# Optimization experiments

Hardware: AMD Instinct MI355X
Metric: run time of the kernel (lower is better)

The kernel has to match this reference:

```python
import jax, jax.numpy as jnp
import numpy as np

ALPHA = 1.0

def setup_inputs() -> dict:
    key = jax.random.key(0)
    k1, k2 = jax.random.split(key)
    B, T, F = 8, 4096, 1024
    x = jax.random.normal(k1, (B, T, F), dtype=jnp.float32)
    # ragged valid lengths in [T//2, T]; mask[b, t] = t < length[b]
    lengths = jax.random.randint(k2, (B,), T // 2, T + 1)
    attention_mask = (jnp.arange(T)[None, :] < lengths[:, None]).astype(jnp.int32)
    return {"input_values": x, "attention_mask": attention_mask}


def reference(input_values, attention_mask):
    # input_values: [B,T,F]; attention_mask: [B,T] (1 for valid, 0 for pad)
    m = attention_mask.astype(input_values.dtype)[..., None]          # [B,T,1]
    L = jnp.sum(m, axis=1)                                            # [B,1]
    # k: per-channel mean over valid timesteps (torch mean over dims [-1,-2])
    k = jnp.sum(input_values * m, axis=1) / L                         # [B,F]
    k_centered = k - jnp.mean(k, axis=-1, keepdims=True)              # [B,F] (center over channels)
    kd = jnp.sqrt(jnp.sum(k_centered ** 2, axis=-1, keepdims=True))   # [B,1]
    # center each timestep over channels
    x_centered = input_values - jnp.mean(input_values, axis=-1, keepdims=True)  # [B,T,F]
    qd = jnp.sqrt(jnp.sum(x_centered ** 2, axis=-1))                  # [B,T]
    num = jnp.einsum('btf,bf->bt', x_centered, k_centered)            # [B,T]
    C_qk = num / (qd * kd)                                            # [B,T]
    A = (1.0 - jax.nn.sigmoid(C_qk)) ** ALPHA                         # [B,T]
    # apply attention and zero out padded positions (original zero-pads)
    out = input_values * A[..., None] * m                             # [B,T,F]
    return out
```

## Files before the change

### kernel.cpp

```cpp
#include <hip/hip_runtime.h>
#include <math.h>

#define BB 8
#define TT 4096
#define FF 1024
#define F4 (FF / 4)
#define TS 128
#define TCHUNK (TT / TS)

typedef float vfloat4 __attribute__((ext_vector_type(4)));

__global__ __launch_bounds__(256) void k1_colsum(const float4* __restrict__ x4,
                                                 const int* __restrict__ mask,
                                                 float* __restrict__ ksum) {
    const int ts  = blockIdx.x;
    const int b   = blockIdx.y;
    const int tid = threadIdx.x;

    const int4* mrow = (const int4*)(mask + (size_t)b * TT + ts * TCHUNK);
    int nv = 0;
    #pragma unroll
    for (int i = 0; i < TCHUNK / 4; ++i) {
        int4 m = mrow[i];
        nv += m.x + m.y + m.z + m.w;
    }
    if (nv == 0) return;

    const float4* xb = x4 + ((size_t)b * TT + (size_t)ts * TCHUNK) * F4 + tid;
    float4 acc = make_float4(0.f, 0.f, 0.f, 0.f);
    #pragma unroll 8
    for (int t = 0; t < nv; ++t) {
        float4 v = xb[(size_t)t * F4];
        acc.x += v.x; acc.y += v.y; acc.z += v.z; acc.w += v.w;
    }

    float* dst = ksum + (size_t)b * FF + tid * 4;
    atomicAdd(dst + 0, acc.x);
    atomicAdd(dst + 1, acc.y);
    atomicAdd(dst + 2, acc.z);
    atomicAdd(dst + 3, acc.w);
}

__global__ __launch_bounds__(256) void k3_apply(const float4* __restrict__ x4,
                                                const int* __restrict__ mask,
                                                const float4* __restrict__ ksum4,
                                                float4* __restrict__ out4) {
    __shared__ float Lred[4];
    const int tid  = threadIdx.x;
    const int wave = tid >> 6;
    const int lane = tid & 63;
    const int b    = blockIdx.y;

    int c = 0;
    #pragma unroll
    for (int i = 0; i < 16; ++i) c += mask[(size_t)b * TT + tid + i * 256];
    float fc = (float)c;
    #pragma unroll
    for (int off = 32; off; off >>= 1) fc += __shfl_xor(fc, off);
    if (lane == 0) Lred[wave] = fc;
    __syncthreads();
    const float Lf   = Lred[0] + Lred[1] + Lred[2] + Lred[3];
    const float invL = 1.0f / Lf;

    const float4* krow = ksum4 + (size_t)b * F4;
    float4 kv[4];
    #pragma unroll
    for (int j = 0; j < 4; ++j) {
        kv[j] = krow[lane + 64 * j];
        kv[j].x *= invL; kv[j].y *= invL; kv[j].z *= invL; kv[j].w *= invL;
    }

    float a = 0.f, q = 0.f;
    #pragma unroll
    for (int j = 0; j < 4; ++j) {
        a += kv[j].x + kv[j].y + kv[j].z + kv[j].w;
        q = fmaf(kv[j].x, kv[j].x, fmaf(kv[j].y, kv[j].y,
            fmaf(kv[j].z, kv[j].z, fmaf(kv[j].w, kv[j].w, q))));
    }
    #pragma unroll
    for (int off = 32; off; off >>= 1) {
        a += __shfl_xor(a, off);
        q += __shfl_xor(q, off);
    }
    const float sk = a;
    const float kd = sqrtf(fmaxf(q - sk * sk * (1.0f / FF), 0.f));

    const int rowbase = blockIdx.x * 16 + wave * 4;
    const size_t base = ((size_t)b * TT + rowbase) * F4;

    const int4 m4 = *(const int4*)(mask + (size_t)b * TT + rowbase);
    const int  nv = m4.x + m4.y + m4.z + m4.w;

    for (int i = nv; i < 4; ++i) {
        vfloat4* orow = (vfloat4*)(out4 + base + (size_t)i * F4);
        vfloat4 z = (vfloat4)(0.f);
        #pragma unroll
        for (int j = 0; j < 4; ++j)
            __builtin_nontemporal_store(z, orow + lane + 64 * j);
    }
    if (nv == 0) return;

    float4 xn[4];
    #pragma unroll
    for (int j = 0; j < 4; ++j) xn[j] = (x4 + base)[lane + 64 * j];

    for (int i = 0; i < nv; ++i) {
        float4 xv[4];
        #pragma unroll
        for (int j = 0; j < 4; ++j) xv[j] = xn[j];
        if (i + 1 < nv) {
            const float4* xrow = x4 + base + (size_t)(i + 1) * F4;
            #pragma unroll
            for (int j = 0; j < 4; ++j) xn[j] = xrow[lane + 64 * j];
        }

        float s1 = 0.f, s2 = 0.f, s3 = 0.f;
        #pragma unroll
        for (int j = 0; j < 4; ++j) {
            s1 += xv[j].x + xv[j].y + xv[j].z + xv[j].w;
            s2 = fmaf(xv[j].x, xv[j].x, fmaf(xv[j].y, xv[j].y,
                 fmaf(xv[j].z, xv[j].z, fmaf(xv[j].w, xv[j].w, s2))));
            s3 = fmaf(xv[j].x, kv[j].x, fmaf(xv[j].y, kv[j].y,
                 fmaf(xv[j].z, kv[j].z, fmaf(xv[j].w, kv[j].w, s3))));
        }
        #pragma unroll
        for (int off = 32; off; off >>= 1) {
            s1 += __shfl_xor(s1, off);
            s2 += __shfl_xor(s2, off);
            s3 += __shfl_xor(s3, off);
        }

        const float mx  = s1 * (1.0f / FF);
        const float num = s3 - mx * sk;
        const float qd  = sqrtf(fmaxf(s2 - s1 * s1 * (1.0f / FF), 0.f));
        const float C   = num / (qd * kd);
        const float A   = 1.0f / (1.0f + __expf(C));

        vfloat4* orow = (vfloat4*)(out4 + base + (size_t)i * F4);
        #pragma unroll
        for (int j = 0; j < 4; ++j) {
            vfloat4 o;
            o.x = xv[j].x * A; o.y = xv[j].y * A;
            o.z = xv[j].z * A; o.w = xv[j].w * A;
            __builtin_nontemporal_store(o, orow + lane + 64 * j);
        }
    }
}

extern "C" void kernel_launch(void* const* d_in, const int* in_sizes, int n_in,
                              void* d_out, int out_size, void* d_ws, size_t ws_size,
                              hipStream_t stream) {
    const float* x    = (const float*)d_in[0];
    const int*   mask = (const int*)d_in[1];
    float*       out  = (float*)d_out;

    float* ksum = (float*)d_ws;

    hipMemsetAsync(ksum, 0, (size_t)BB * FF * sizeof(float), stream);

    k1_colsum<<<dim3(TS, BB), 256, 0, stream>>>((const float4*)x, mask, ksum);
    k3_apply<<<dim3(TT / 16, BB), 256, 0, stream>>>((const float4*)x, mask,
                                                    (const float4*)ksum,
                                                    (float4*)out);
}
```

Baseline: 247.7 us.

## Move padded-row zeroing and length count into the colsum kernel

The first kernel gains extra blocks. They write zeros to the padded output rows, and one extra block per batch counts the valid length and stores it to workspace. The zero stores can then overlap with the column-sum reads instead of sitting in the apply kernel. The apply kernel drops its per-block 4K-element mask reduction and the barrier that followed it. Blocks with no valid rows now exit before loading k, at the cost of one more workspace read per block.

```diff
diff --git a/kernel.cpp b/kernel.cpp
--- a/kernel.cpp
+++ b/kernel.cpp
@@ -7,60 +7,92 @@
 #define F4 (FF / 4)
 #define TS 128
 #define TCHUNK (TT / TS)
+#define ZB (TT / 16)
 
 typedef float vfloat4 __attribute__((ext_vector_type(4)));
 
 __global__ __launch_bounds__(256) void k1_colsum(const float4* __restrict__ x4,
                                                  const int* __restrict__ mask,
-                                                 float* __restrict__ ksum) {
-    const int ts  = blockIdx.x;
+                                                 float* __restrict__ ksum,
+                                                 float* __restrict__ Lf,
+                                                 float4* __restrict__ out4) {
+    const int bx  = blockIdx.x;
     const int b   = blockIdx.y;
     const int tid = threadIdx.x;
 
-    const int4* mrow = (const int4*)(mask + (size_t)b * TT + ts * TCHUNK);
-    int nv = 0;
-    #pragma unroll
-    for (int i = 0; i < TCHUNK / 4; ++i) {
-        int4 m = mrow[i];
-        nv += m.x + m.y + m.z + m.w;
-    }
-    if (nv == 0) return;
+    if (bx < TS) {
+        const int4* mrow = (const int4*)(mask + (size_t)b * TT + bx * TCHUNK);
+        int nv = 0;
+        #pragma unroll
+        for (int i = 0; i < TCHUNK / 4; ++i) {
+            int4 m = mrow[i];
+            nv += m.x + m.y + m.z + m.w;
+        }
+        if (nv == 0) return;
 
-    const float4* xb = x4 + ((size_t)b * TT + (size_t)ts * TCHUNK) * F4 + tid;
-    float4 acc = make_float4(0.f, 0.f, 0.f, 0.f);
-    #pragma unroll 8
-    for (int t = 0; t < nv; ++t) {
-        float4 v = xb[(size_t)t * F4];
-        acc.x += v.x; acc.y += v.y; acc.z += v.z; acc.w += v.w;
+        const float4* xb = x4 + ((size_t)b * TT + (size_t)bx * TCHUNK) * F4 + tid;
+        float4 acc = make_float4(0.f, 0.f, 0.f, 0.f);
+        #pragma unroll 8
+        for (int t = 0; t < nv; ++t) {
+            float4 v = xb[(size_t)t * F4];
+            acc.x += v.x; acc.y += v.y; acc.z += v.z; acc.w += v.w;
+        }
+        float* dst = ksum + (size_t)b * FF + tid * 4;
+        atomicAdd(dst + 0, acc.x);
+        atomicAdd(dst + 1, acc.y);
+        atomicAdd(dst + 2, acc.z);
+        atomicAdd(dst + 3, acc.w);
+        return;
     }
 
-    float* dst = ksum + (size_t)b * FF + tid * 4;
-    atomicAdd(dst + 0, acc.x);
-    atomicAdd(dst + 1, acc.y);
-    atomicAdd(dst + 2, acc.z);
-    atomicAdd(dst + 3, acc.w);
+    if (bx < TS + ZB) {
+        const int wave = tid >> 6;
+        const int lane = tid & 63;
+        const int rowbase = (bx - TS) * 16 + wave * 4;
+        const int4 m4 = *(const int4*)(mask + (size_t)b * TT + rowbase);
+        const int  nv = m4.x + m4.y + m4.z + m4.w;
+        const size_t base = ((size_t)b * TT + rowbase) * F4;
+        for (int i = nv; i < 4; ++i) {
+            vfloat4* orow = (vfloat4*)(out4 + base + (size_t)i * F4);
+            vfloat4 z = (vfloat4)(0.f);
+            #pragma unroll
+            for (int j = 0; j < 4; ++j)
+                __builtin_nontemporal_store(z, orow + lane + 64 * j);
+        }
+        return;
+    }
+
+    {
+        __shared__ float Lred[4];
+        const int wave = tid >> 6;
+        const int lane = tid & 63;
+        int c = 0;
+        #pragma unroll
+        for (int i = 0; i < 16; ++i) c += mask[(size_t)b * TT + tid + i * 256];
+        float fc = (float)c;
+        #pragma unroll
+        for (int off = 32; off; off >>= 1) fc += __shfl_xor(fc, off);
+        if (lane == 0) Lred[wave] = fc;
+        __syncthreads();
+        if (tid == 0) Lf[b] = Lred[0] + Lred[1] + Lred[2] + Lred[3];
+    }
 }
 
 __global__ __launch_bounds__(256) void k3_apply(const float4* __restrict__ x4,
                                                 const int* __restrict__ mask,
                                                 const float4* __restrict__ ksum4,
+                                                const float* __restrict__ Lf,
                                                 float4* __restrict__ out4) {
-    __shared__ float Lred[4];
-    const int tid  = threadIdx.x;
-    const int wave = tid >> 6;
-    const int lane = tid & 63;
+    const int wave = threadIdx.x >> 6;
+    const int lane = threadIdx.x & 63;
     const int b    = blockIdx.y;
+    const int rowbase = blockIdx.x * 16 + wave * 4;
 
-    int c = 0;
-    #pragma unroll
-    for (int i = 0; i < 16; ++i) c += mask[(size_t)b * TT + tid + i * 256];
-    float fc = (float)c;
-    #pragma unroll
-    for (int off = 32; off; off >>= 1) fc += __shfl_xor(fc, off);
-    if (lane == 0) Lred[wave] = fc;
-    __syncthreads();
-    const float Lf   = Lred[0] + Lred[1] + Lred[2] + Lred[3];
-    const float invL = 1.0f / Lf;
+    const int4 m4 = *(const int4*)(mask + (size_t)b * TT + rowbase);
+    const int  nv = m4.x + m4.y + m4.z + m4.w;
+    if (nv == 0) return;
+
+    const float invL = 1.0f / Lf[b];
 
     const float4* krow = ksum4 + (size_t)b * F4;
     float4 kv[4];
@@ -85,21 +117,7 @@
     const float sk = a;
     const float kd = sqrtf(fmaxf(q - sk * sk * (1.0f / FF), 0.f));
 
-    const int rowbase = blockIdx.x * 16 + wave * 4;
     const size_t base = ((size_t)b * TT + rowbase) * F4;
-
-    const int4 m4 = *(const int4*)(mask + (size_t)b * TT + rowbase);
-    const int  nv = m4.x + m4.y + m4.z + m4.w;
-
-    for (int i = nv; i < 4; ++i) {
-        vfloat4* orow = (vfloat4*)(out4 + base + (size_t)i * F4);
-        vfloat4 z = (vfloat4)(0.f);
-        #pragma unroll
-        for (int j = 0; j < 4; ++j)
-            __builtin_nontemporal_store(z, orow + lane + 64 * j);
-    }
-    if (nv == 0) return;
-
     float4 xn[4];
     #pragma unroll
     for (int j = 0; j < 4; ++j) xn[j] = (x4 + base)[lane + 64 * j];
@@ -155,11 +173,13 @@
     float*       out  = (float*)d_out;
 
     float* ksum = (float*)d_ws;
+    float* Lf   = ksum + (size_t)BB * FF;
 
     hipMemsetAsync(ksum, 0, (size_t)BB * FF * sizeof(float), stream);
 
-    k1_colsum<<<dim3(TS, BB), 256, 0, stream>>>((const float4*)x, mask, ksum);
+    k1_colsum<<<dim3(TS + ZB + 1, BB), 256, 0, stream>>>((const float4*)x, mask,
+                                                         ksum, Lf, (float4*)out);
     k3_apply<<<dim3(TT / 16, BB), 256, 0, stream>>>((const float4*)x, mask,
-                                                    (const float4*)ksum,
+                                                    (const float4*)ksum, Lf,
                                                     (float4*)out);
 }
```

New measurement: 251.8 us. About the same (+1.7%).
